# Kernel tuning notes

Measured on AMD Instinct MI355X. Metric: run time of the kernel, lower is better.

## Reference

```python
import jax, jax.numpy as jnp
import numpy as np

NODE_DIM = 128
INSTR_DIM = 128
HIDDEN_DIM = 256
N_NODES = 50000
N_EDGES = 800000
N_GRAPHS = 64


def setup_inputs() -> dict:
    key = jax.random.key(0)
    k_instr, k_x, k_ei, k_b, k_w1, k_b1, k_w2, k_b2 = jax.random.split(key, 8)
    instr = jax.random.normal(k_instr, (N_GRAPHS, INSTR_DIM), dtype=jnp.float32)
    x = jax.random.normal(k_x, (N_NODES, NODE_DIM), dtype=jnp.float32)
    edge_index = jax.random.randint(k_ei, (2, N_EDGES), 0, N_NODES, dtype=jnp.int64)
    batch = jnp.sort(jax.random.randint(k_b, (N_NODES,), 0, N_GRAPHS, dtype=jnp.int64))
    in_dim = 2 * NODE_DIM + INSTR_DIM  # 384
    lim1 = 1.0 / np.sqrt(in_dim)
    lim2 = 1.0 / np.sqrt(HIDDEN_DIM)
    W1 = jax.random.uniform(k_w1, (in_dim, HIDDEN_DIM), jnp.float32, -lim1, lim1)
    b1 = jax.random.uniform(k_b1, (HIDDEN_DIM,), jnp.float32, -lim1, lim1)
    W2 = jax.random.uniform(k_w2, (HIDDEN_DIM, 1), jnp.float32, -lim2, lim2)
    b2 = jax.random.uniform(k_b2, (1,), jnp.float32, -lim2, lim2)
    return {"instr": instr, "x": x, "edge_index": edge_index, "batch": batch,
            "W1": W1, "b1": b1, "W2": W2, "b2": b2}


def reference(instr, x, edge_index, batch, W1, b1, W2, b2):
    src, dst = edge_index[0], edge_index[1]
    u = instr[batch[src]]                       # [E, Di] gather via batch[src]
    h = jnp.concatenate([x[src], x[dst], u], axis=-1)  # [E, 2D+Di]
    h = jax.nn.silu(h @ W1 + b1)                # [E, H] (dropout p=0 -> identity)
    logits = (h @ W2 + b2).squeeze(-1)          # [E]
    return logits
```

## Files before the change

kernel.cpp:

```cpp
#include <hip/hip_runtime.h>
#include <hip/hip_bf16.h>
#include <stdint.h>

#define E_EDGES   800000
#define N_NODES_C 50000
#define NG        64
#define DD        128
#define HH        256
#define KDIM      384

typedef __bf16 bf16x8 __attribute__((ext_vector_type(8)));
typedef __bf16 bf16x4 __attribute__((ext_vector_type(4)));
typedef float  f32x4  __attribute__((ext_vector_type(4)));

__device__ __forceinline__ void gld16(const void* g, void* l) {
  __builtin_amdgcn_global_load_lds(
      (__attribute__((address_space(1))) void*)g,
      (__attribute__((address_space(3))) void*)l, 16, 0, 0);
}

__global__ void k_cvt4(const float* __restrict__ in, __bf16* __restrict__ out, int n4) {
  int i = blockIdx.x * blockDim.x + threadIdx.x;
  if (i < n4) {
    float4 v = ((const float4*)in)[i];
    bf16x4 b;
    b[0] = (__bf16)v.x; b[1] = (__bf16)v.y; b[2] = (__bf16)v.z; b[3] = (__bf16)v.w;
    ((bf16x4*)out)[i] = b;
  }
}

__global__ void k_w1pt(const float* __restrict__ w1, __bf16* __restrict__ w1pt) {
  int idx = blockIdx.x * blockDim.x + threadIdx.x;
  if (idx < 512 * 128) {
    int n = idx >> 7;
    int k = idx & 127;
    float v = (n < 256) ? w1[k * HH + n] : w1[(128 + k) * HH + (n - 256)];
    w1pt[n * 128 + k] = (__bf16)v;
  }
}

__global__ void k_r2(const float* __restrict__ instr, const float* __restrict__ w1,
                     const float* __restrict__ b1, float* __restrict__ r2) {
  __shared__ float ins[DD];
  int g = blockIdx.x;
  int c = threadIdx.x;
  if (c < DD) ins[c] = instr[g * DD + c];
  __syncthreads();
  float sum = b1[c];
#pragma unroll 8
  for (int k = 0; k < DD; ++k) sum += ins[k] * w1[(256 + k) * HH + c];
  r2[g * HH + c] = sum;
}

__launch_bounds__(512, 4)
__global__ void k_nodegemm(const __bf16* __restrict__ xbf,
                           const __bf16* __restrict__ w1pt,
                           __bf16* __restrict__ pq)
{
  __shared__ __align__(16) char smem[16384 + 32768];
  char* As = smem;
  char* Bs = smem + 16384;

  const int tid  = threadIdx.x;
  const int lane = tid & 63;
  const int wid  = tid >> 6;
  const int rowbase = blockIdx.x * 128;
  const int nt      = blockIdx.y;

  const int arow  = tid >> 2;
  const int aslot = tid & 3;
  const int akap  = aslot ^ ((arow >> 1) & 3);
  int gr = rowbase + arow; if (gr >= N_NODES_C) gr = N_NODES_C - 1;
  const char* aptr = (const char*)xbf + (size_t)gr * 256 + akap * 16;

  const char* bptr[2];
#pragma unroll
  for (int it = 0; it < 2; ++it) {
    int j2 = tid + it * 512;
    int n  = j2 >> 2;
    int bk = (j2 & 3) ^ ((n >> 1) & 3);
    bptr[it] = (const char*)w1pt + (size_t)(nt * 256 + n) * 256 + bk * 16;
  }

  char* ldsA = As + wid * 1024;
  char* ldsB = Bs + wid * 1024;

  auto stage = [&](int cur, int kk) {
    gld16(bptr[0] + kk * 64, ldsB + cur * 16384);
    gld16(bptr[1] + kk * 64, ldsB + cur * 16384 + 8192);
    gld16(aptr    + kk * 64, ldsA + cur * 8192);
  };

  const int wm    = wid >> 2;
  const int wn    = wid & 3;
  const int l15   = lane & 15;
  const int kap_r = (lane >> 4) ^ ((l15 >> 1) & 3);
  const int aoff  = wm * 4096 + l15 * 64 + kap_r * 16;
  const int boff  = wn * 4096 + l15 * 64 + kap_r * 16;

  f32x4 acc[4][4];
#pragma unroll
  for (int mi = 0; mi < 4; ++mi)
#pragma unroll
    for (int ni = 0; ni < 4; ++ni)
      acc[mi][ni] = f32x4{0.f, 0.f, 0.f, 0.f};

  stage(0, 0);

  for (int kk = 0; kk < 4; ++kk) {
    const int cur = kk & 1;
    __syncthreads();
    if (kk + 1 < 4) stage(cur ^ 1, kk + 1);

    const char* pA = As + cur * 8192;
    const char* pB = Bs + cur * 16384;
    bf16x8 av[4], bv[4];
#pragma unroll
    for (int mi = 0; mi < 4; ++mi) av[mi] = *(const bf16x8*)(pA + aoff + mi * 1024);
#pragma unroll
    for (int ni = 0; ni < 4; ++ni) bv[ni] = *(const bf16x8*)(pB + boff + ni * 1024);
#pragma unroll
    for (int mi = 0; mi < 4; ++mi)
#pragma unroll
      for (int ni = 0; ni < 4; ++ni)
        acc[mi][ni] = __builtin_amdgcn_mfma_f32_16x16x32_bf16(av[mi], bv[ni], acc[mi][ni], 0, 0, 0);
  }

  const int rg = lane >> 4;
#pragma unroll
  for (int mi = 0; mi < 4; ++mi) {
    int row = rowbase + wm * 64 + mi * 16 + rg * 4;
#pragma unroll
    for (int r = 0; r < 4; ++r) {
      if (row + r < N_NODES_C) {
        size_t base = (size_t)(row + r) * 512 + nt * 256 + wn * 64 + l15;
#pragma unroll
        for (int ni = 0; ni < 4; ++ni)
          pq[base + ni * 16] = (__bf16)acc[mi][ni][r];
      }
    }
  }
}

__launch_bounds__(256, 8)
__global__ void k_edge(const __bf16* __restrict__ pq,
                       const float* __restrict__ r2,
                       const int*   __restrict__ ei,
                       const int*   __restrict__ batch,
                       const float* __restrict__ w2,
                       const float* __restrict__ b2,
                       float* __restrict__ out)
{
  const int tid  = threadIdx.x;
  const int lane = tid & 63;
  const int wid  = tid >> 6;
  const int half = lane >> 5;
  const int l    = lane & 31;
  const int c0   = l * 8;

  float w2r[8];
  {
    float4 a = *(const float4*)(w2 + c0);
    float4 b = *(const float4*)(w2 + c0 + 4);
    w2r[0]=a.x; w2r[1]=a.y; w2r[2]=a.z; w2r[3]=a.w;
    w2r[4]=b.x; w2r[5]=b.y; w2r[6]=b.z; w2r[7]=b.w;
  }
  const float bb = b2[0];

  for (int e = blockIdx.x * 8 + wid * 2 + half; e < E_EDGES; e += gridDim.x * 8) {
    int s = ei[e];
    int d = ei[E_EDGES + e];
    int g = batch[s];

    bf16x8 pv = *(const bf16x8*)(pq + (size_t)s * 512 + c0);
    bf16x8 qv = *(const bf16x8*)(pq + (size_t)d * 512 + 256 + c0);
    float4 r0 = *(const float4*)(r2 + g * HH + c0);
    float4 r1 = *(const float4*)(r2 + g * HH + c0 + 4);
    float rv[8] = {r0.x, r0.y, r0.z, r0.w, r1.x, r1.y, r1.z, r1.w};

    float sum = 0.f;
#pragma unroll
    for (int j = 0; j < 8; ++j) {
      float v  = (float)pv[j] + (float)qv[j] + rv[j];
      float sv = v * __builtin_amdgcn_rcpf(1.0f + __expf(-v));
      sum += sv * w2r[j];
    }
#pragma unroll
    for (int off = 1; off < 32; off <<= 1)
      sum += __shfl_xor(sum, off, 64);
    if (l == 0) out[e] = sum + bb;
  }
}

#define BM 128
#define KSTEPS 12
#define THREADS 512

template <int MODE>
__launch_bounds__(THREADS, 4)
__global__ void k_main(const float* __restrict__ xf,
                       const float* __restrict__ instrf,
                       const int*   __restrict__ ei,
                       const int*   __restrict__ batch,
                       const __bf16* __restrict__ xbf,
                       const __bf16* __restrict__ insbf,
                       const __bf16* __restrict__ w1t,
                       const float* __restrict__ b1,
                       const float* __restrict__ w2,
                       const float* __restrict__ b2,
                       float* __restrict__ out)
{
  __shared__ __align__(16) char smem[16384 + 32768 + 2048];
  char*  As  = smem;
  char*  Bs  = smem + 16384;
  float* red = (float*)(smem + 16384 + 32768);

  const int tid  = threadIdx.x;
  const int lane = tid & 63;
  const int wid  = tid >> 6;
  const int blk  = blockIdx.x;

  const int arow  = tid >> 2;
  const int aslot = tid & 3;
  const int akap  = aslot ^ ((arow >> 1) & 3);
  const int e     = blk * BM + arow;
  const int s     = ei[e];
  const int d     = ei[E_EDGES + e];
  const int g     = batch[s];

  const char  *aS = nullptr, *aD = nullptr, *aI = nullptr;
  const float *fS = nullptr, *fD = nullptr, *fI = nullptr;
  if (MODE == 0) {
    aS = (const char*)xbf   + s * 256 + akap * 16;
    aD = (const char*)xbf   + d * 256 + akap * 16;
    aI = (const char*)insbf + g * 256 + akap * 16;
  } else {
    fS = xf     + s * DD + akap * 8;
    fD = xf     + d * DD + akap * 8;
    fI = instrf + g * DD + akap * 8;
  }

  const char* bptr[2];
#pragma unroll
  for (int it = 0; it < 2; ++it) {
    int j2 = tid + it * 512;
    int n  = j2 >> 2;
    int bk = (j2 & 3) ^ ((n >> 1) & 3);
    bptr[it] = (const char*)w1t + n * (KDIM * 2) + bk * 16;
  }

  char* ldsA = As + wid * 1024;
  char* ldsB = Bs + wid * 1024;

  auto stage = [&](int cur, int kk) {
    gld16(bptr[0] + kk * 64, ldsB + cur * 16384);
    gld16(bptr[1] + kk * 64, ldsB + cur * 16384 + 8192);
    if (MODE == 0) {
      const char* ga = (kk < 4) ? (aS + kk * 64)
                     : (kk < 8) ? (aD + (kk - 4) * 64)
                                : (aI + (kk - 8) * 64);
      gld16(ga, ldsA + cur * 8192);
    } else {
      const float* gf = (kk < 4) ? (fS + kk * 32)
                      : (kk < 8) ? (fD + (kk - 4) * 32)
                                 : (fI + (kk - 8) * 32);
      float4 v0 = *(const float4*)gf;
      float4 v1 = *(const float4*)(gf + 4);
      bf16x8 bv;
      bv[0] = (__bf16)v0.x; bv[1] = (__bf16)v0.y; bv[2] = (__bf16)v0.z; bv[3] = (__bf16)v0.w;
      bv[4] = (__bf16)v1.x; bv[5] = (__bf16)v1.y; bv[6] = (__bf16)v1.z; bv[7] = (__bf16)v1.w;
      *(bf16x8*)(As + cur * 8192 + tid * 16) = bv;
    }
  };

  const int wm    = wid >> 2;
  const int wn    = wid & 3;
  const int l15   = lane & 15;
  const int kap_r = (lane >> 4) ^ ((l15 >> 1) & 3);
  const int aoff  = wm * 4096 + l15 * 64 + kap_r * 16;
  const int boff  = wn * 4096 + l15 * 64 + kap_r * 16;

  f32x4 acc[4][4];
#pragma unroll
  for (int mi = 0; mi < 4; ++mi)
#pragma unroll
    for (int ni = 0; ni < 4; ++ni)
      acc[mi][ni] = f32x4{0.f, 0.f, 0.f, 0.f};

  stage(0, 0);

  for (int kk = 0; kk < KSTEPS; ++kk) {
    const int cur = kk & 1;
    __syncthreads();
    if (kk + 1 < KSTEPS) stage(cur ^ 1, kk + 1);

    const char* pA = As + cur * 8192;
    const char* pB = Bs + cur * 16384;
    bf16x8 av[4], bv[4];
#pragma unroll
    for (int mi = 0; mi < 4; ++mi) av[mi] = *(const bf16x8*)(pA + aoff + mi * 1024);
#pragma unroll
    for (int ni = 0; ni < 4; ++ni) bv[ni] = *(const bf16x8*)(pB + boff + ni * 1024);
#pragma unroll
    for (int mi = 0; mi < 4; ++mi)
#pragma unroll
      for (int ni = 0; ni < 4; ++ni)
        acc[mi][ni] = __builtin_amdgcn_mfma_f32_16x16x32_bf16(av[mi], bv[ni], acc[mi][ni], 0, 0, 0);
  }

  float b1c[4], w2c[4];
#pragma unroll
  for (int ni = 0; ni < 4; ++ni) {
    int n = wn * 64 + ni * 16 + l15;
    b1c[ni] = b1[n];
    w2c[ni] = w2[n];
  }

  float rowsum[4][4];
#pragma unroll
  for (int mi = 0; mi < 4; ++mi)
#pragma unroll
    for (int r = 0; r < 4; ++r) rowsum[mi][r] = 0.f;

#pragma unroll
  for (int ni = 0; ni < 4; ++ni) {
    float bb = b1c[ni], ww = w2c[ni];
#pragma unroll
    for (int mi = 0; mi < 4; ++mi)
#pragma unroll
      for (int r = 0; r < 4; ++r) {
        float v  = acc[mi][ni][r] + bb;
        float sv = v / (1.0f + __expf(-v));
        rowsum[mi][r] += sv * ww;
      }
  }

#pragma unroll
  for (int off = 1; off < 16; off <<= 1)
#pragma unroll
    for (int mi = 0; mi < 4; ++mi)
#pragma unroll
      for (int r = 0; r < 4; ++r)
        rowsum[mi][r] += __shfl_xor(rowsum[mi][r], off, 64);

  if (l15 == 0) {
    int rg = lane >> 4;
#pragma unroll
    for (int mi = 0; mi < 4; ++mi)
#pragma unroll
      for (int r = 0; r < 4; ++r)
        red[wn * 128 + wm * 64 + mi * 16 + rg * 4 + r] = rowsum[mi][r];
  }
  __syncthreads();

  if (tid < BM) {
    float v = red[tid] + red[128 + tid] + red[256 + tid] + red[384 + tid] + b2[0];
    out[blk * BM + tid] = v;
  }
}

extern "C" void kernel_launch(void* const* d_in, const int* in_sizes, int n_in,
                              void* d_out, int out_size, void* d_ws, size_t ws_size,
                              hipStream_t stream) {
  const float* instr = (const float*)d_in[0];
  const float* x     = (const float*)d_in[1];
  const int*   ei    = (const int*)d_in[2];
  const int*   batch = (const int*)d_in[3];
  const float* W1    = (const float*)d_in[4];
  const float* b1    = (const float*)d_in[5];
  const float* W2    = (const float*)d_in[6];
  const float* b2    = (const float*)d_in[7];
  float* out = (float*)d_out;
  char* ws = (char*)d_ws;

  const size_t off_xbf  = 0;
  const size_t off_w1pt = 12800000;
  const size_t off_r2   = 12931072;
  const size_t off_pq   = 12996608;
  const size_t need_full = 64196608;

  if (ws_size >= need_full) {
    __bf16* xbf  = (__bf16*)(ws + off_xbf);
    __bf16* w1pt = (__bf16*)(ws + off_w1pt);
    float*  r2   = (float*)(ws + off_r2);
    __bf16* pq   = (__bf16*)(ws + off_pq);

    k_cvt4<<<(N_NODES_C * DD / 4 + 255) / 256, 256, 0, stream>>>(x, xbf, N_NODES_C * DD / 4);
    k_w1pt<<<(512 * 128 + 255) / 256, 256, 0, stream>>>(W1, w1pt);
    k_r2<<<NG, HH, 0, stream>>>(instr, W1, b1, r2);
    dim3 g1((N_NODES_C + 127) / 128, 2);
    k_nodegemm<<<g1, 512, 0, stream>>>(xbf, w1pt, pq);
    k_edge<<<2048, 256, 0, stream>>>(pq, r2, ei, batch, W2, b2, out);
    return;
  }

  const size_t f_off_xbf = 0;
  const size_t f_off_ins = 12800000;
  const size_t f_off_w1t = 12816384;
  const size_t need_fast = 13012992;

  if (ws_size >= need_fast) {
    __bf16* xbf   = (__bf16*)(ws + f_off_xbf);
    __bf16* insbf = (__bf16*)(ws + f_off_ins);
    __bf16* w1t   = (__bf16*)(ws + f_off_w1t);
    k_cvt4<<<(N_NODES_C * DD / 4 + 255) / 256, 256, 0, stream>>>(x, xbf, N_NODES_C * DD / 4);
    k_cvt4<<<(NG * DD / 4 + 255) / 256, 256, 0, stream>>>(instr, insbf, NG * DD / 4);
    {
    }
    extern __global__ void k_w1t_fb(const float*, __bf16*);
    k_w1t_fb<<<(KDIM * HH + 255) / 256, 256, 0, stream>>>(W1, w1t);
    k_main<0><<<E_EDGES / BM, THREADS, 0, stream>>>(x, instr, ei, batch, xbf, insbf, w1t,
                                                    b1, W2, b2, out);
  } else {
    __bf16* w1t = (__bf16*)ws;
    extern __global__ void k_w1t_fb(const float*, __bf16*);
    k_w1t_fb<<<(KDIM * HH + 255) / 256, 256, 0, stream>>>(W1, w1t);
    k_main<1><<<E_EDGES / BM, THREADS, 0, stream>>>(x, instr, ei, batch, nullptr, nullptr, w1t,
                                                    b1, W2, b2, out);
  }
}

__global__ void k_w1t_fb(const float* __restrict__ w1, __bf16* __restrict__ w1t) {
  int idx = blockIdx.x * blockDim.x + threadIdx.x;
  if (idx < KDIM * HH) {
    int k = idx >> 8;
    int n = idx & 255;
    w1t[n * KDIM + k] = (__bf16)w1[idx];
  }
}
```

Measured before the change: 156.0 us.

## Fold per-graph instruction term into node GEMM and fuse prep kernels

The three preprocessing kernels (x conversion, W1 transpose, r2 per-graph bias) are merged into one launch. The per-graph r2 term is added into the source-side P output during the node GEMM, so the edge kernel no longer loads batch[s] or r2. The edge kernel also handles two edges per half-wave, unpacks bf16 by bit shifts, and computes SiLU with exp2 and one shared reciprocal for each pair of values. The intent is to cut launch overhead, a dependent gather, and transcendental cost, at the price of adding r2 to P before rounding to bf16, which slightly changes precision.

```diff
diff --git a/kernel.cpp b/kernel.cpp
--- a/kernel.cpp
+++ b/kernel.cpp
@@ -12,6 +12,7 @@
 typedef __bf16 bf16x8 __attribute__((ext_vector_type(8)));
 typedef __bf16 bf16x4 __attribute__((ext_vector_type(4)));
 typedef float  f32x4  __attribute__((ext_vector_type(4)));
+typedef uint32_t u32x4 __attribute__((ext_vector_type(4)));
 
 __device__ __forceinline__ void gld16(const void* g, void* l) {
   __builtin_amdgcn_global_load_lds(
@@ -19,42 +20,49 @@
       (__attribute__((address_space(3))) void*)l, 16, 0, 0);
 }
 
-__global__ void k_cvt4(const float* __restrict__ in, __bf16* __restrict__ out, int n4) {
-  int i = blockIdx.x * blockDim.x + threadIdx.x;
-  if (i < n4) {
-    float4 v = ((const float4*)in)[i];
+__device__ __forceinline__ float bf_hi(uint32_t u) { return __uint_as_float(u & 0xffff0000u); }
+__device__ __forceinline__ float bf_lo(uint32_t u) { return __uint_as_float(u << 16); }
+
+#define PREP_CVT_BLKS 6250
+#define PREP_W1_BLKS  256
+#define PREP_R2_BLKS  64
+
+__global__ void k_prep(const float* __restrict__ x, const float* __restrict__ w1,
+                       const float* __restrict__ instr, const float* __restrict__ b1,
+                       __bf16* __restrict__ xbf, __bf16* __restrict__ w1pt,
+                       float* __restrict__ r2) {
+  __shared__ float ins[DD];
+  const int bid = blockIdx.x;
+  const int tid = threadIdx.x;
+  if (bid < PREP_CVT_BLKS) {
+    int i = bid * 256 + tid;
+    float4 v = ((const float4*)x)[i];
     bf16x4 b;
     b[0] = (__bf16)v.x; b[1] = (__bf16)v.y; b[2] = (__bf16)v.z; b[3] = (__bf16)v.w;
-    ((bf16x4*)out)[i] = b;
-  }
-}
-
-__global__ void k_w1pt(const float* __restrict__ w1, __bf16* __restrict__ w1pt) {
-  int idx = blockIdx.x * blockDim.x + threadIdx.x;
-  if (idx < 512 * 128) {
+    ((bf16x4*)xbf)[i] = b;
+  } else if (bid < PREP_CVT_BLKS + PREP_W1_BLKS) {
+    int idx = (bid - PREP_CVT_BLKS) * 256 + tid;
     int n = idx >> 7;
     int k = idx & 127;
     float v = (n < 256) ? w1[k * HH + n] : w1[(128 + k) * HH + (n - 256)];
     w1pt[n * 128 + k] = (__bf16)v;
-  }
-}
-
-__global__ void k_r2(const float* __restrict__ instr, const float* __restrict__ w1,
-                     const float* __restrict__ b1, float* __restrict__ r2) {
-  __shared__ float ins[DD];
-  int g = blockIdx.x;
-  int c = threadIdx.x;
-  if (c < DD) ins[c] = instr[g * DD + c];
-  __syncthreads();
-  float sum = b1[c];
+  } else {
+    int g = bid - (PREP_CVT_BLKS + PREP_W1_BLKS);
+    int c = tid;
+    if (c < DD) ins[c] = instr[g * DD + c];
+    __syncthreads();
+    float sum = b1[c];
 #pragma unroll 8
-  for (int k = 0; k < DD; ++k) sum += ins[k] * w1[(256 + k) * HH + c];
-  r2[g * HH + c] = sum;
+    for (int k = 0; k < DD; ++k) sum += ins[k] * w1[(256 + k) * HH + c];
+    r2[g * HH + c] = sum;
+  }
 }
 
 __launch_bounds__(512, 4)
 __global__ void k_nodegemm(const __bf16* __restrict__ xbf,
                            const __bf16* __restrict__ w1pt,
+                           const int*   __restrict__ batch,
+                           const float* __restrict__ r2,
                            __bf16* __restrict__ pq)
 {
   __shared__ __align__(16) char smem[16384 + 32768];
@@ -127,16 +135,25 @@
   }
 
   const int rg = lane >> 4;
+  const bool fold = (nt == 0);
 #pragma unroll
   for (int mi = 0; mi < 4; ++mi) {
     int row = rowbase + wm * 64 + mi * 16 + rg * 4;
 #pragma unroll
     for (int r = 0; r < 4; ++r) {
-      if (row + r < N_NODES_C) {
-        size_t base = (size_t)(row + r) * 512 + nt * 256 + wn * 64 + l15;
+      int rr = row + r;
+      if (rr < N_NODES_C) {
+        float addv[4] = {0.f, 0.f, 0.f, 0.f};
+        if (fold) {
+          int g = batch[rr];
+          const float* r2row = r2 + g * HH + wn * 64 + l15;
+#pragma unroll
+          for (int ni = 0; ni < 4; ++ni) addv[ni] = r2row[ni * 16];
+        }
+        size_t base = (size_t)rr * 512 + nt * 256 + wn * 64 + l15;
 #pragma unroll
         for (int ni = 0; ni < 4; ++ni)
-          pq[base + ni * 16] = (__bf16)acc[mi][ni][r];
+          pq[base + ni * 16] = (__bf16)(acc[mi][ni][r] + addv[ni]);
       }
     }
   }
@@ -144,9 +161,7 @@
 
 __launch_bounds__(256, 8)
 __global__ void k_edge(const __bf16* __restrict__ pq,
-                       const float* __restrict__ r2,
                        const int*   __restrict__ ei,
-                       const int*   __restrict__ batch,
                        const float* __restrict__ w2,
                        const float* __restrict__ b2,
                        float* __restrict__ out)
@@ -166,35 +181,71 @@
     w2r[4]=b.x; w2r[5]=b.y; w2r[6]=b.z; w2r[7]=b.w;
   }
   const float bb = b2[0];
-
-  for (int e = blockIdx.x * 8 + wid * 2 + half; e < E_EDGES; e += gridDim.x * 8) {
-    int s = ei[e];
-    int d = ei[E_EDGES + e];
-    int g = batch[s];
-
-    bf16x8 pv = *(const bf16x8*)(pq + (size_t)s * 512 + c0);
-    bf16x8 qv = *(const bf16x8*)(pq + (size_t)d * 512 + 256 + c0);
-    float4 r0 = *(const float4*)(r2 + g * HH + c0);
-    float4 r1 = *(const float4*)(r2 + g * HH + c0 + 4);
-    float rv[8] = {r0.x, r0.y, r0.z, r0.w, r1.x, r1.y, r1.z, r1.w};
-
-    float sum = 0.f;
-#pragma unroll
-    for (int j = 0; j < 8; ++j) {
-      float v  = (float)pv[j] + (float)qv[j] + rv[j];
-      float sv = v * __builtin_amdgcn_rcpf(1.0f + __expf(-v));
-      sum += sv * w2r[j];
+  const float NL2E = -1.44269504f;
+
+  for (int e = blockIdx.x * 16 + (wid * 2 + half) * 2; e < E_EDGES; e += gridDim.x * 16) {
+    int s0 = ei[e];     int d0 = ei[E_EDGES + e];
+    int s1 = ei[e + 1]; int d1 = ei[E_EDGES + e + 1];
+
+    u32x4 p0 = *(const u32x4*)(pq + (size_t)s0 * 512 + c0);
+    u32x4 q0 = *(const u32x4*)(pq + (size_t)d0 * 512 + 256 + c0);
+    u32x4 p1 = *(const u32x4*)(pq + (size_t)s1 * 512 + c0);
+    u32x4 q1 = *(const u32x4*)(pq + (size_t)d1 * 512 + 256 + c0);
+
+    float sum0 = 0.f, sum1 = 0.f;
+#pragma unroll
+    for (int k = 0; k < 4; ++k) {
+      {
+        float va = bf_lo(p0[k]) + bf_lo(q0[k]);
+        float vb = bf_hi(p0[k]) + bf_hi(q0[k]);
+        float ta = __builtin_amdgcn_exp2f(va * NL2E);
+        float tb = __builtin_amdgcn_exp2f(vb * NL2E);
+        float da = 1.f + ta, db = 1.f + tb;
+        float rc = __builtin_amdgcn_rcpf(da * db);
+        sum0 += (va * w2r[2 * k]) * (rc * db) + (vb * w2r[2 * k + 1]) * (rc * da);
+      }
+      {
+        float va = bf_lo(p1[k]) + bf_lo(q1[k]);
+        float vb = bf_hi(p1[k]) + bf_hi(q1[k]);
+        float ta = __builtin_amdgcn_exp2f(va * NL2E);
+        float tb = __builtin_amdgcn_exp2f(vb * NL2E);
+        float da = 1.f + ta, db = 1.f + tb;
+        float rc = __builtin_amdgcn_rcpf(da * db);
+        sum1 += (va * w2r[2 * k]) * (rc * db) + (vb * w2r[2 * k + 1]) * (rc * da);
+      }
     }
-#pragma unroll
-    for (int off = 1; off < 32; off <<= 1)
-      sum += __shfl_xor(sum, off, 64);
-    if (l == 0) out[e] = sum + bb;
+
+#pragma unroll
+    for (int off = 1; off < 32; off <<= 1) {
+      sum0 += __shfl_xor(sum0, off, 64);
+      sum1 += __shfl_xor(sum1, off, 64);
+    }
+    if (l == 0) *(float2*)(out + e) = make_float2(sum0 + bb, sum1 + bb);
   }
 }
 
 #define BM 128
 #define KSTEPS 12
 #define THREADS 512
+
+__global__ void k_cvt4(const float* __restrict__ in, __bf16* __restrict__ out, int n4) {
+  int i = blockIdx.x * blockDim.x + threadIdx.x;
+  if (i < n4) {
+    float4 v = ((const float4*)in)[i];
+    bf16x4 b;
+    b[0] = (__bf16)v.x; b[1] = (__bf16)v.y; b[2] = (__bf16)v.z; b[3] = (__bf16)v.w;
+    ((bf16x4*)out)[i] = b;
+  }
+}
+
+__global__ void k_w1t_fb(const float* __restrict__ w1, __bf16* __restrict__ w1t) {
+  int idx = blockIdx.x * blockDim.x + threadIdx.x;
+  if (idx < KDIM * HH) {
+    int k = idx >> 8;
+    int n = idx & 255;
+    w1t[n * KDIM + k] = (__bf16)w1[idx];
+  }
+}
 
 template <int MODE>
 __launch_bounds__(THREADS, 4)
@@ -324,12 +375,12 @@
 
 #pragma unroll
   for (int ni = 0; ni < 4; ++ni) {
-    float bb = b1c[ni], ww = w2c[ni];
+    float bbv = b1c[ni], ww = w2c[ni];
 #pragma unroll
     for (int mi = 0; mi < 4; ++mi)
 #pragma unroll
       for (int r = 0; r < 4; ++r) {
-        float v  = acc[mi][ni][r] + bb;
+        float v  = acc[mi][ni][r] + bbv;
         float sv = v / (1.0f + __expf(-v));
         rowsum[mi][r] += sv * ww;
       }
@@ -385,12 +436,11 @@
     float*  r2   = (float*)(ws + off_r2);
     __bf16* pq   = (__bf16*)(ws + off_pq);
 
-    k_cvt4<<<(N_NODES_C * DD / 4 + 255) / 256, 256, 0, stream>>>(x, xbf, N_NODES_C * DD / 4);
-    k_w1pt<<<(512 * 128 + 255) / 256, 256, 0, stream>>>(W1, w1pt);
-    k_r2<<<NG, HH, 0, stream>>>(instr, W1, b1, r2);
+    k_prep<<<PREP_CVT_BLKS + PREP_W1_BLKS + PREP_R2_BLKS, 256, 0, stream>>>(
+        x, W1, instr, b1, xbf, w1pt, r2);
     dim3 g1((N_NODES_C + 127) / 128, 2);
-    k_nodegemm<<<g1, 512, 0, stream>>>(xbf, w1pt, pq);
-    k_edge<<<2048, 256, 0, stream>>>(pq, r2, ei, batch, W2, b2, out);
+    k_nodegemm<<<g1, 512, 0, stream>>>(xbf, w1pt, batch, r2, pq);
+    k_edge<<<2048, 256, 0, stream>>>(pq, ei, W2, b2, out);
     return;
   }
 
@@ -405,26 +455,13 @@
     __bf16* w1t   = (__bf16*)(ws + f_off_w1t);
     k_cvt4<<<(N_NODES_C * DD / 4 + 255) / 256, 256, 0, stream>>>(x, xbf, N_NODES_C * DD / 4);
     k_cvt4<<<(NG * DD / 4 + 255) / 256, 256, 0, stream>>>(instr, insbf, NG * DD / 4);
-    {
-    }
-    extern __global__ void k_w1t_fb(const float*, __bf16*);
     k_w1t_fb<<<(KDIM * HH + 255) / 256, 256, 0, stream>>>(W1, w1t);
     k_main<0><<<E_EDGES / BM, THREADS, 0, stream>>>(x, instr, ei, batch, xbf, insbf, w1t,
                                                     b1, W2, b2, out);
   } else {
     __bf16* w1t = (__bf16*)ws;
-    extern __global__ void k_w1t_fb(const float*, __bf16*);
     k_w1t_fb<<<(KDIM * HH + 255) / 256, 256, 0, stream>>>(W1, w1t);
     k_main<1><<<E_EDGES / BM, THREADS, 0, stream>>>(x, instr, ei, batch, nullptr, nullptr, w1t,
                                                     b1, W2, b2, out);
   }
 }
-
-__global__ void k_w1t_fb(const float* __restrict__ w1, __bf16* __restrict__ w1t) {
-  int idx = blockIdx.x * blockDim.x + threadIdx.x;
-  if (idx < KDIM * HH) {
-    int k = idx >> 8;
-    int n = idx & 255;
-    w1t[n * KDIM + k] = (__bf16)w1[idx];
-  }
-}
```

Result: faster. 150.2 us (-3.7%).
